# Performance work log

Measured on AMD Instinct MI355X. Metric: run time of the kernel, lower is better.

Reference implementation:

```python
import jax, jax.numpy as jnp
import numpy as np

B, C, H, W = 4, 512, 48, 48
DQ = C // 8  # inter_rate = 8
N = H * W
EPS = 1e-5


def _local_mask(radius):
    r = np.arange(N) // W
    c = np.arange(N) % W
    d = np.maximum(np.abs(r[:, None] - r[None, :]), np.abs(c[:, None] - c[None, :]))
    return jnp.asarray(d <= radius)


def setup_inputs() -> dict:
    key = jax.random.key(0)
    ks = jax.random.split(key, 12)
    def nrm(k, shape, scale=0.04):
        return jax.random.normal(k, shape, dtype=jnp.float32) * scale
    zc = jnp.zeros((C,), jnp.float32)
    oc = jnp.ones((C,), jnp.float32)
    return {
        "x": jax.random.normal(ks[0], (B, C, H, W), dtype=jnp.float32),
        "Wq": nrm(ks[1], (DQ, C)), "bq": jnp.zeros((DQ,), jnp.float32),
        "Wk": nrm(ks[2], (DQ, C)), "bk": jnp.zeros((DQ,), jnp.float32),
        "Wv": nrm(ks[3], (C, C)), "bv": zc,
        "conv1_w": nrm(ks[4], (C, C, 3, 3)),
        "bn1_w": oc, "bn1_b": zc, "bn1_m": zc, "bn1_v": oc,
        "conv2_w": nrm(ks[5], (C, C, 3, 3)),
        "bn2_w": oc, "bn2_b": zc, "bn2_m": zc, "bn2_v": oc,
        "sig1_w": nrm(ks[6], (C, C)), "sig1_b": zc,
        "sig2_w": nrm(ks[7], (C, C)), "sig2_b": zc,
        "gamma": jnp.full((1,), 0.5, jnp.float32),
        "gamma1": jnp.full((1,), 0.3, jnp.float32),
        "gamma2": jnp.full((1,), 0.2, jnp.float32),
        "mask1": _local_mask(6),
        "mask2": _local_mask(12),
    }


def _masked_softmax(e, mask):
    # exp(e)*mask / sum(exp(e)*mask) == softmax with -inf outside mask
    e = e - jnp.max(e, axis=-1, keepdims=True)
    w = jnp.exp(e) * mask.astype(e.dtype)
    return w / jnp.sum(w, axis=-1, keepdims=True)


def _conv1x1(t, w, b):
    return jnp.einsum('bchw,dc->bdhw', t, w) + b[None, :, None, None]


def _conv3x3_bn_relu(t, w, g, beta, mu, var):
    y = jax.lax.conv_general_dilated(t, w, (1, 1), 'SAME',
                                     dimension_numbers=('NCHW', 'OIHW', 'NCHW'))
    scale = (g / jnp.sqrt(var + EPS))[None, :, None, None]
    y = (y - mu[None, :, None, None]) * scale + beta[None, :, None, None]
    return jax.nn.relu(y)


def _forward(x, Wq, bq, Wk, bk, Wv, bv, conv1_w, bn1_w, bn1_b, bn1_m, bn1_v,
             conv2_w, bn2_w, bn2_b, bn2_m, bn2_v, sig1_w, sig1_b, sig2_w, sig2_b,
             gamma, gamma1, gamma2, mask1, mask2):
    b, c, h, w = x.shape
    n = h * w
    q = _conv1x1(x, Wq, bq).reshape(b, -1, n)   # [B, d, N]
    k = _conv1x1(x, Wk, bk).reshape(b, -1, n)   # [B, d, N]
    energy = jnp.einsum('bdn,bdm->bnm', q, k)   # [B, N, N] (query rows)
    a0 = jax.nn.softmax(energy, axis=-1)
    a1 = _masked_softmax(energy, mask1)
    a2 = _masked_softmax(energy, mask2)
    v = _conv1x1(x, Wv, bv).reshape(b, c, n)
    # torch: bmm(value, attention.permute(0,2,1)) -> out[b,c,m] = sum_n v[b,c,n]*a[m,n]
    out0 = jnp.einsum('bcn,bmn->bcm', v, a0).reshape(b, c, h, w)
    out0 = gamma * out0 + x
    out0 = _conv3x3_bn_relu(out0, conv1_w, bn1_w, bn1_b, bn1_m, bn1_v)
    s1 = (jax.nn.sigmoid(_conv1x1(out0, sig1_w, sig1_b)) * out0).reshape(b, c, n)
    out1 = jnp.einsum('bcn,bmn->bcm', s1, a1).reshape(b, c, h, w)
    out1 = gamma1 * out1 + out0
    out1 = _conv3x3_bn_relu(out1, conv2_w, bn2_w, bn2_b, bn2_m, bn2_v)
    s2 = (jax.nn.sigmoid(_conv1x1(out1, sig2_w, sig2_b)) * out1).reshape(b, c, n)
    out2 = jnp.einsum('bcn,bmn->bcm', s2, a2).reshape(b, c, h, w)
    return gamma2 * out2 + out1


def reference(x, Wq, bq, Wk, bk, Wv, bv, conv1_w, bn1_w, bn1_b, bn1_m, bn1_v,
              conv2_w, bn2_w, bn2_b, bn2_m, bn2_v, sig1_w, sig1_b, sig2_w, sig2_b,
              gamma, gamma1, gamma2, mask1, mask2):
    return _forward(x, Wq, bq, Wk, bk, Wv, bv, conv1_w, bn1_w, bn1_b, bn1_m, bn1_v,
                    conv2_w, bn2_w, bn2_b, bn2_m, bn2_v, sig1_w, sig1_b, sig2_w, sig2_b,
                    gamma, gamma1, gamma2, mask1, mask2)
```

## Files before the change

### kernel.cpp

```cpp
#include <hip/hip_runtime.h>
#include <math.h>

#define BB 4
#define CC 512
#define HH 48
#define WW 48
#define NN 2304
#define DDQ 64
#define LDSP 72
#define PW 50
#define PROWS 2500

typedef __attribute__((ext_vector_type(4))) float f32x4;
typedef __attribute__((ext_vector_type(8))) _Float16 half8;
typedef __attribute__((ext_vector_type(4))) _Float16 half4;
typedef __attribute__((ext_vector_type(8))) short bf16x8;

__device__ __forceinline__ int imax(int a, int b) { return a > b ? a : b; }
__device__ __forceinline__ int imin(int a, int b) { return a < b ? a : b; }
__device__ __forceinline__ int prow(int m) {
    int h = m / WW, w = m - h * WW;
    return (h + 1) * PW + (w + 1);
}
__device__ __forceinline__ unsigned short f2bf(float f) {
    unsigned u = __float_as_uint(f);
    u += 0x7fffu + ((u >> 16) & 1u);
    return (unsigned short)(u >> 16);
}
__device__ __forceinline__ float bf2f(unsigned short s) {
    unsigned u = ((unsigned)s) << 16;
    return __uint_as_float(u);
}

typedef __attribute__((address_space(1))) unsigned int g_u32;
typedef __attribute__((address_space(3))) unsigned int l_u32;
__device__ __forceinline__ void gl16(const void* g, void* l) {
    __builtin_amdgcn_global_load_lds((const g_u32*)g, (l_u32*)l, 16, 0, 0);
}

#define WAIT6()  asm volatile("s_waitcnt vmcnt(6)" ::: "memory")
#define WAIT0()  asm volatile("s_waitcnt vmcnt(0)" ::: "memory")
#define BAR()    { __builtin_amdgcn_s_barrier(); asm volatile("" ::: "memory"); }

#define BIG_DECODE()                                          \
    int raw = blockIdx.x;                                     \
    int wg = ((raw & 7) * 72) + (raw >> 3);                   \
    int jx = wg % 36; int rem = wg / 36;                      \
    int j0 = jx * 64, i0 = (rem & 3) * 128, b = rem >> 2;

#define BWAVE_IDX()                                  \
    int tid = threadIdx.x;                           \
    int wave = tid >> 6, lane = tid & 63;            \
    int wm = (wave >> 1) * 64, wn = (wave & 1) * 32; \
    int x = lane & 15, qq = lane >> 4;

__device__ __forceinline__ half8 fragld(const _Float16* T, int r, int c) {
    int kb = c ^ (r & 7);
    return *(const half8*)(T + r * 64 + kb * 8);
}
__device__ __forceinline__ bf16x8 fragld_b(const unsigned short* T, int r, int c) {
    int kb = c ^ (r & 7);
    return *(const bf16x8*)(T + r * 64 + kb * 8);
}

__device__ __forceinline__ void btile(const _Float16* As, const _Float16* Bs,
                                      f32x4 acc[4][2], int wm, int wn, int x, int qq) {
#pragma unroll
    for (int ks = 0; ks < 2; ++ks) {
        int c = ks * 4 + qq;
        half8 a0 = fragld(As, wm + x, c);
        half8 a1 = fragld(As, wm + 16 + x, c);
        half8 a2 = fragld(As, wm + 32 + x, c);
        half8 a3 = fragld(As, wm + 48 + x, c);
        half8 b0 = fragld(Bs, wn + x, c);
        half8 b1 = fragld(Bs, wn + 16 + x, c);
        acc[0][0] = __builtin_amdgcn_mfma_f32_16x16x32_f16(a0, b0, acc[0][0], 0, 0, 0);
        acc[0][1] = __builtin_amdgcn_mfma_f32_16x16x32_f16(a0, b1, acc[0][1], 0, 0, 0);
        acc[1][0] = __builtin_amdgcn_mfma_f32_16x16x32_f16(a1, b0, acc[1][0], 0, 0, 0);
        acc[1][1] = __builtin_amdgcn_mfma_f32_16x16x32_f16(a1, b1, acc[1][1], 0, 0, 0);
        acc[2][0] = __builtin_amdgcn_mfma_f32_16x16x32_f16(a2, b0, acc[2][0], 0, 0, 0);
        acc[2][1] = __builtin_amdgcn_mfma_f32_16x16x32_f16(a2, b1, acc[2][1], 0, 0, 0);
        acc[3][0] = __builtin_amdgcn_mfma_f32_16x16x32_f16(a3, b0, acc[3][0], 0, 0, 0);
        acc[3][1] = __builtin_amdgcn_mfma_f32_16x16x32_f16(a3, b1, acc[3][1], 0, 0, 0);
    }
}
__device__ __forceinline__ void btile_b(const unsigned short* As, const unsigned short* Bs,
                                        f32x4 acc[4][2], int wm, int wn, int x, int qq) {
#pragma unroll
    for (int ks = 0; ks < 2; ++ks) {
        int c = ks * 4 + qq;
        bf16x8 a0 = fragld_b(As, wm + x, c);
        bf16x8 a1 = fragld_b(As, wm + 16 + x, c);
        bf16x8 a2 = fragld_b(As, wm + 32 + x, c);
        bf16x8 a3 = fragld_b(As, wm + 48 + x, c);
        bf16x8 b0 = fragld_b(Bs, wn + x, c);
        bf16x8 b1 = fragld_b(Bs, wn + 16 + x, c);
        acc[0][0] = __builtin_amdgcn_mfma_f32_16x16x32_bf16(a0, b0, acc[0][0], 0, 0, 0);
        acc[0][1] = __builtin_amdgcn_mfma_f32_16x16x32_bf16(a0, b1, acc[0][1], 0, 0, 0);
        acc[1][0] = __builtin_amdgcn_mfma_f32_16x16x32_bf16(a1, b0, acc[1][0], 0, 0, 0);
        acc[1][1] = __builtin_amdgcn_mfma_f32_16x16x32_bf16(a1, b1, acc[1][1], 0, 0, 0);
        acc[2][0] = __builtin_amdgcn_mfma_f32_16x16x32_bf16(a2, b0, acc[2][0], 0, 0, 0);
        acc[2][1] = __builtin_amdgcn_mfma_f32_16x16x32_bf16(a2, b1, acc[2][1], 0, 0, 0);
        acc[3][0] = __builtin_amdgcn_mfma_f32_16x16x32_bf16(a3, b0, acc[3][0], 0, 0, 0);
        acc[3][1] = __builtin_amdgcn_mfma_f32_16x16x32_bf16(a3, b1, acc[3][1], 0, 0, 0);
    }
}

#define BACC_INIT()                                         \
    f32x4 zf = {0.f, 0.f, 0.f, 0.f};                        \
    f32x4 acc[4][2];                                        \
    _Pragma("unroll") for (int i_ = 0; i_ < 4; ++i_) {      \
        acc[i_][0] = zf; acc[i_][1] = zf; }

#define SLOT_A(i) int sb = (wave * 4 + (i)) * 64; int s = sb + lane; \
                  int r = s >> 3, kb = s & 7; int koff = ((kb ^ (r & 7)) << 3);
#define SLOT_B(i) int sb = (wave * 2 + (i)) * 64; int s = sb + lane; \
                  int r = s >> 3, kb = s & 7; int koff = ((kb ^ (r & 7)) << 3);

__device__ __forceinline__ void stage_rows(_Float16* dst, const _Float16* __restrict__ src,
                                           int ld, int row0, int k0, int tid) {
#pragma unroll
    for (int i = 0; i < 2; ++i) {
        int s = tid * 2 + i;
        int r = s >> 3, off = (s & 7) << 3;
        *(half8*)(dst + r * LDSP + off) =
            *(const half8*)(src + (size_t)(row0 + r) * ld + k0 + off);
    }
}
__device__ __forceinline__ void mfma_tile(const _Float16* As, const _Float16* Bs,
                                          f32x4 acc[2][2], int wm, int wn, int x, int qq) {
#pragma unroll
    for (int ks = 0; ks < 2; ++ks) {
        int kof = ks * 32 + qq * 8;
        half8 a0 = *(const half8*)(As + (wm + x) * LDSP + kof);
        half8 a1 = *(const half8*)(As + (wm + 16 + x) * LDSP + kof);
        half8 b0 = *(const half8*)(Bs + (wn + x) * LDSP + kof);
        half8 b1 = *(const half8*)(Bs + (wn + 16 + x) * LDSP + kof);
        acc[0][0] = __builtin_amdgcn_mfma_f32_16x16x32_f16(a0, b0, acc[0][0], 0, 0, 0);
        acc[0][1] = __builtin_amdgcn_mfma_f32_16x16x32_f16(a0, b1, acc[0][1], 0, 0, 0);
        acc[1][0] = __builtin_amdgcn_mfma_f32_16x16x32_f16(a1, b0, acc[1][0], 0, 0, 0);
        acc[1][1] = __builtin_amdgcn_mfma_f32_16x16x32_f16(a1, b1, acc[1][1], 0, 0, 0);
    }
}
#define WAVE_IDX()                             \
    int tid = threadIdx.x;                     \
    int wave = tid >> 6, lane = tid & 63;      \
    int wm = (wave >> 1) * 32, wn = (wave & 1) * 32; \
    int x = lane & 15, qq = lane >> 4;
#define ACC_INIT()                             \
    f32x4 zf = {0.f, 0.f, 0.f, 0.f};           \
// ... 59 lines not shown
    _Float16* outT = blockIdx.y ? kT : qT;
    const _Float16* xTb = xT + (size_t)b * NN * CC;
    ACC_INIT();
    for (int kc = 0; kc < CC; kc += 64) {
        stage_rows(As, Wp, CC, 0, kc, tid);
        stage_rows(Bs, xTb, CC, j0, kc, tid);
        __syncthreads();
        mfma_tile(As, Bs, acc, wm, wn, x, qq);
        __syncthreads();
    }
#pragma unroll
    for (int ms = 0; ms < 2; ++ms) {
        int R0 = wm + ms * 16 + qq * 4;
#pragma unroll
        for (int ns = 0; ns < 2; ++ns) {
            int Ccol = j0 + wn + ns * 16 + x;
            half4 t;
            t.x = (_Float16)(acc[ms][ns][0] + bias[R0 + 0]);
            t.y = (_Float16)(acc[ms][ns][1] + bias[R0 + 1]);
            t.z = (_Float16)(acc[ms][ns][2] + bias[R0 + 2]);
            t.w = (_Float16)(acc[ms][ns][3] + bias[R0 + 3]);
            *(half4*)(outT + ((size_t)b * NN + Ccol) * DDQ + R0) = t;
        }
    }
}

template <int EPI, int PAD>
__global__ __launch_bounds__(256) void k_cgemm(const _Float16* __restrict__ W,
                                               const float* __restrict__ bias,
                                               const _Float16* __restrict__ Bsrc,
                                               const _Float16* __restrict__ gateH,
                                               unsigned short* __restrict__ out) {
    __shared__ __align__(16) _Float16 As[2][128 * 64];
    __shared__ __align__(16) _Float16 Bs[2][64 * 64];
    BWAVE_IDX();
    BIG_DECODE();
    const _Float16* Bb = Bsrc + (size_t)b * (PAD ? (size_t)PROWS * CC : (size_t)NN * CC);

    const _Float16* aSrc[4]; int aOf[4];
#pragma unroll
    for (int i = 0; i < 4; ++i) {
        SLOT_A(i);
        aSrc[i] = W + (size_t)(i0 + r) * CC + koff;
        aOf[i] = sb * 8;
    }
    const _Float16* bSrc[2]; int bOf[2];
#pragma unroll
    for (int i = 0; i < 2; ++i) {
        SLOT_B(i);
        int row = PAD ? prow(j0 + r) : (j0 + r);
        bSrc[i] = Bb + (size_t)row * CC + koff;
        bOf[i] = sb * 8;
    }
    BACC_INIT();
#define STG_G(kc, nb)                                                          \
    { _Pragma("unroll") for (int i = 0; i < 4; ++i)                            \
          gl16(aSrc[i] + (kc), As[nb] + aOf[i]);                               \
      _Pragma("unroll") for (int i = 0; i < 2; ++i)                            \
          gl16(bSrc[i] + (kc), Bs[nb] + bOf[i]); }
    STG_G(0, 0);
    STG_G(64, 1);
    const int NSTEP = CC / 64;
#pragma unroll
    for (int t = 0; t + 2 < NSTEP; ++t) {
        WAIT6();
        BAR();
        btile(As[t & 1], Bs[t & 1], acc, wm, wn, x, qq);
        BAR();
        STG_G((t + 2) * 64, (t & 1));
    }
    WAIT6();
    BAR();
    btile(As[(NSTEP - 2) & 1], Bs[(NSTEP - 2) & 1], acc, wm, wn, x, qq);
    WAIT0();
    BAR();
    btile(As[(NSTEP - 1) & 1], Bs[(NSTEP - 1) & 1], acc, wm, wn, x, qq);
#undef STG_G
#pragma unroll
    for (int mt = 0; mt < 4; ++mt) {
        int R0 = i0 + wm + mt * 16 + qq * 4;
#pragma unroll
        for (int nt = 0; nt < 2; ++nt) {
            int Ccol = j0 + wn + nt * 16 + x;
            half4 gh;
            if (EPI == 1)
                gh = *(const half4*)(gateH + ((size_t)b * PROWS + prow(Ccol)) * CC + R0);
#pragma unroll
            for (int e = 0; e < 4; ++e) {
                float v = acc[mt][nt][e] + bias[R0 + e];
                size_t idx = ((size_t)b * CC + R0 + e) * NN + Ccol;
                if (EPI == 1) v = (float)gh[e] / (1.f + __expf(-v));
                out[idx] = f2bf(v);
            }
        }
    }
}

__global__ __launch_bounds__(256) void k_exp(const _Float16* __restrict__ qT,
                                             const _Float16* __restrict__ kT,
                                             unsigned short* __restrict__ attnB,
                                             float* __restrict__ rowsum, int rad) {
    __shared__ _Float16 qs[64 * LDSP];
    __shared__ _Float16 ks[64 * LDSP];
    __shared__ unsigned short Eh[64 * 72];
    __shared__ float psum[512];
    WAVE_IDX();
    int j0 = blockIdx.x * 64, i0 = blockIdx.y * 64, b = blockIdx.z;
    if (rad > 0) {
        int hlo = i0 / WW, hhi = (i0 + 63) / WW;
        int h2lo = imax(0, hlo - rad), h2hi = imin(HH - 1, hhi + rad);
        int klo = (h2lo * WW) & ~63;
        int khi = imin(NN, ((h2hi + 1) * WW + 63) & ~63);
        if (j0 + 64 <= klo || j0 >= khi) return;
    }
    stage_rows(qs, qT + (size_t)b * NN * DDQ, DDQ, i0, 0, tid);
    stage_rows(ks, kT + (size_t)b * NN * DDQ, DDQ, j0, 0, tid);
    __syncthreads();
    ACC_INIT();
    mfma_tile(qs, ks, acc, wm, wn, x, qq);
#pragma unroll
    for (int ns = 0; ns < 2; ++ns) {
        int col = wn + ns * 16 + x;
        int gn = j0 + col;
        int hn = gn / WW, cn = gn % WW;
#pragma unroll
        for (int ms = 0; ms < 2; ++ms)
#pragma unroll
            for (int e = 0; e < 4; ++e) {
                int row = wm + ms * 16 + qq * 4 + e;
                int gm = i0 + row;
                bool valid = true;
                if (rad > 0) {
                    int dh = gm / WW - hn; if (dh < 0) dh = -dh;
                    int dc = gm % WW - cn; if (dc < 0) dc = -dc;
                    valid = (dh <= rad) && (dc <= rad);
                }
                float w = valid ? __expf(acc[ms][ns][e]) : 0.f;
                Eh[row * 72 + col] = f2bf(w);
            }
    }
    __syncthreads();
#pragma unroll
    for (int t = 0; t < 2; ++t) {
        int s = tid + t * 256;
        int r = s >> 3, cg = (s & 7) << 3;
        bf16x8 v = *(const bf16x8*)(Eh + r * 72 + cg);
        *(bf16x8*)(attnB + ((size_t)b * NN + i0 + r) * NN + j0 + cg) = v;
        float ss = 0.f;
#pragma unroll
        for (int j = 0; j < 8; ++j) ss += bf2f((unsigned short)v[j]);
        psum[s] = ss;
    }
    __syncthreads();
    if (tid < 64) {
        float tot = 0.f;
#pragma unroll
        for (int g = 0; g < 8; ++g) tot += psum[tid * 8 + g];
        atomicAdd(rowsum + (size_t)b * NN + i0 + tid, tot);
    }
}

__global__ __launch_bounds__(256) void k_attn(const unsigned short* __restrict__ A,
                                              const unsigned short* __restrict__ attnB,
                                              const float* __restrict__ rowsum,
                                              const float* __restrict__ resF,
                                              const _Float16* __restrict__ resH,
                                              const float* __restrict__ gamma,
                                              float* __restrict__ outF,
                                              _Float16* __restrict__ outT, int rad) {
    __shared__ __align__(16) unsigned short As[2][128 * 64];
    __shared__ __align__(16) unsigned short Bs[2][64 * 64];
    BWAVE_IDX();
    BIG_DECODE();
    int klo = 0, khi = NN;
    if (rad > 0) {
        int hlo = j0 / WW, hhi = (j0 + 63) / WW;
        int h2lo = imax(0, hlo - rad), h2hi = imin(HH - 1, hhi + rad);
        klo = (h2lo * WW) & ~63;
        khi = imin(NN, ((h2hi + 1) * WW + 63) & ~63);
    }
    const unsigned short* Ab = A + (size_t)b * CC * NN;
    const unsigned short* Tb = attnB + (size_t)b * NN * NN;

    const unsigned short* aSrc[4]; int aOf[4];
#pragma unroll
    for (int i = 0; i < 4; ++i) {
        SLOT_A(i);
        aSrc[i] = Ab + (size_t)(i0 + r) * NN + koff + klo;
        aOf[i] = sb * 8;
    }
    const unsigned short* bSrc[2]; int bOf[2];
#pragma unroll
    for (int i = 0; i < 2; ++i) {
        SLOT_B(i);
        bSrc[i] = Tb + (size_t)(j0 + r) * NN + koff + klo;
        bOf[i] = sb * 8;
    }
    BACC_INIT();
    int nsteps = (khi - klo) >> 6;
#define STG_T(kc, nb)                                                          \
    { _Pragma("unroll") for (int i = 0; i < 4; ++i)                            \
          gl16(aSrc[i] + (kc), As[nb] + aOf[i]);                               \
      _Pragma("unroll") for (int i = 0; i < 2; ++i)                            \
          gl16(bSrc[i] + (kc), Bs[nb] + bOf[i]); }
    STG_T(0, 0);
    STG_T(64, 1);
    for (int t = 0; t + 2 < nsteps; ++t) {
        WAIT6();
        BAR();
        btile_b(As[t & 1], Bs[t & 1], acc, wm, wn, x, qq);
        BAR();
        STG_T((t + 2) << 6, (t & 1));
    }
    WAIT6();
    BAR();
    btile_b(As[(nsteps - 2) & 1], Bs[(nsteps - 2) & 1], acc, wm, wn, x, qq);
    WAIT0();
    BAR();
    btile_b(As[(nsteps - 1) & 1], Bs[(nsteps - 1) & 1], acc, wm, wn, x, qq);
#undef STG_T
    float g = gamma[0];
#pragma unroll
    for (int mt = 0; mt < 4; ++mt) {
        int R0 = i0 + wm + mt * 16 + qq * 4;
#pragma unroll
        for (int nt = 0; nt < 2; ++nt) {
            int Ccol = j0 + wn + nt * 16 + x;
            float linv = g / fmaxf(rowsum[(size_t)b * NN + Ccol], 1e-30f);
            float v[4];
            if (resH) {
                half4 rh = *(const half4*)(resH + ((size_t)b * PROWS + prow(Ccol)) * CC + R0);
#pragma unroll
                for (int e = 0; e < 4; ++e)
                    v[e] = acc[mt][nt][e] * linv + (float)rh[e];
            } else {
#pragma unroll
                for (int e = 0; e < 4; ++e)
                    v[e] = acc[mt][nt][e] * linv + resF[((size_t)b * CC + R0 + e) * NN + Ccol];
            }
            if (outT) {
                half4 t;
                t.x = (_Float16)v[0]; t.y = (_Float16)v[1];
                t.z = (_Float16)v[2]; t.w = (_Float16)v[3];
                *(half4*)(outT + ((size_t)b * PROWS + prow(Ccol)) * CC + R0) = t;
            }
            if (outF) {
#pragma unroll
                for (int e = 0; e < 4; ++e)
                    outF[((size_t)b * CC + R0 + e) * NN + Ccol] = v[e];
            }
        }
    }
}

__global__ __launch_bounds__(256) void k_conv3(const _Float16* __restrict__ Arep,
                                               const _Float16* __restrict__ Tpad,
                                               const float* __restrict__ bng,
                                               const float* __restrict__ bnb,
                                               const float* __restrict__ bnm,
                                               const float* __restrict__ bnv,
                                               float* __restrict__ outF,
                                               _Float16* __restrict__ outT) {
    __shared__ __align__(16) _Float16 As[2][128 * 64];
    __shared__ __align__(16) _Float16 Bs[2][64 * 64];
    BWAVE_IDX();
    BIG_DECODE();
    const _Float16* Tb = Tpad + (size_t)b * PROWS * CC;

    const _Float16* aBase[4]; int aOf[4];
#pragma unroll
    for (int i = 0; i < 4; ++i) {
        SLOT_A(i);
        aBase[i] = Arep + (size_t)(i0 + r) * CC + koff;
        aOf[i] = sb * 8;
    }
    const _Float16* bBase[2]; int bOf[2];
#pragma unroll
    for (int i = 0; i < 2; ++i) {
        SLOT_B(i);
        bBase[i] = Tb + (size_t)prow(j0 + r) * CC + koff;
        bOf[i] = sb * 8;
    }
    BACC_INIT();

#define STAGE_CONV(u, nb)                                                       \
    {                                                                           \
        int rt_ = (u) >> 3, ci_ = ((u) & 7) << 6;                               \
        int r3_ = rt_ / 3;                                                      \
        ptrdiff_t aoff_ = (ptrdiff_t)rt_ * (CC * CC) + ci_;                     \
        ptrdiff_t boff_ =                                                       \
            (ptrdiff_t)((r3_ - 1) * PW + (rt_ - r3_ * 3 - 1)) * CC + ci_;       \
        _Pragma("unroll") for (int i = 0; i < 4; ++i)                           \
            gl16(aBase[i] + aoff_, As[nb] + aOf[i]);                            \
        _Pragma("unroll") for (int i = 0; i < 2; ++i)                           \
            gl16(bBase[i] + boff_, Bs[nb] + bOf[i]);                            \
    }

    STAGE_CONV(0, 0);
    STAGE_CONV(1, 1);
    const int TOT = 9 * (CC / 64);
#pragma unroll 2
    for (int t = 0; t + 2 < TOT; ++t) {
        WAIT6();
        BAR();
        btile(As[t & 1], Bs[t & 1], acc, wm, wn, x, qq);
        BAR();
        STAGE_CONV(t + 2, (t & 1));
    }
    WAIT6();
    BAR();
    btile(As[(TOT - 2) & 1], Bs[(TOT - 2) & 1], acc, wm, wn, x, qq);
    WAIT0();
    BAR();
    btile(As[(TOT - 1) & 1], Bs[(TOT - 1) & 1], acc, wm, wn, x, qq);
#undef STAGE_CONV

#pragma unroll
    for (int mt = 0; mt < 4; ++mt) {
        int R0 = i0 + wm + mt * 16 + qq * 4;
        float sc[4], sh[4];
#pragma unroll
        for (int e = 0; e < 4; ++e) {
            sc[e] = bng[R0 + e] * rsqrtf(bnv[R0 + e] + 1e-5f);
            sh[e] = bnb[R0 + e] - bnm[R0 + e] * sc[e];
        }
#pragma unroll
        for (int nt = 0; nt < 2; ++nt) {
            int Ccol = j0 + wn + nt * 16 + x;
            float v[4];
#pragma unroll
            for (int e = 0; e < 4; ++e) {
                float t = acc[mt][nt][e] * sc[e] + sh[e];
                v[e] = t > 0.f ? t : 0.f;
            }
            if (outF) {
#pragma unroll
                for (int e = 0; e < 4; ++e)
                    outF[((size_t)b * CC + R0 + e) * NN + Ccol] = v[e];
            }
            half4 t4;
            t4.x = (_Float16)v[0]; t4.y = (_Float16)v[1];
            t4.z = (_Float16)v[2]; t4.w = (_Float16)v[3];
            *(half4*)(outT + ((size_t)b * PROWS + prow(Ccol)) * CC + R0) = t4;
        }
    }
}

extern "C" void kernel_launch(void* const* d_in, const int* in_sizes, int n_in,
                              void* d_out, int out_size, void* d_ws, size_t ws_size,
                              hipStream_t stream) {
    const float* xin  = (const float*)d_in[0];
    const float* Wq   = (const float*)d_in[1];
    const float* bq   = (const float*)d_in[2];
    const float* Wk   = (const float*)d_in[3];
    const float* bk   = (const float*)d_in[4];
    const float* Wv   = (const float*)d_in[5];
    const float* bv   = (const float*)d_in[6];
    const float* c1w  = (const float*)d_in[7];
    const float* bn1w = (const float*)d_in[8];
    const float* bn1b = (const float*)d_in[9];
    const float* bn1m = (const float*)d_in[10];
    const float* bn1v = (const float*)d_in[11];
    const float* c2w  = (const float*)d_in[12];
    const float* bn2w = (const float*)d_in[13];
    const float* bn2b = (const float*)d_in[14];
    const float* bn2m = (const float*)d_in[15];
    const float* bn2v = (const float*)d_in[16];
    const float* s1w  = (const float*)d_in[17];
    const float* s1b  = (const float*)d_in[18];
    const float* s2w  = (const float*)d_in[19];
    const float* s2b  = (const float*)d_in[20];
    const float* gamma  = (const float*)d_in[21];
    const float* gamma1 = (const float*)d_in[22];
    const float* gamma2 = (const float*)d_in[23];

    float* out = (float*)d_out;

    char* p = (char*)d_ws;
    unsigned short* attn = (unsigned short*)p; p += (size_t)BB * NN * NN * 2;
    _Float16* xT    = (_Float16*)p; p += (size_t)BB * NN * CC * 2;
    _Float16* qT    = (_Float16*)p; p += (size_t)BB * NN * DDQ * 2;
    _Float16* kT    = (_Float16*)p; p += (size_t)BB * NN * DDQ * 2;
    unsigned short* vsB = (unsigned short*)p; p += (size_t)BB * CC * NN * 2;
    _Float16* TattnP= (_Float16*)p; p += (size_t)BB * PROWS * CC * 2;
    _Float16* TconvP= (_Float16*)p; p += (size_t)BB * PROWS * CC * 2;
    float*    rR    = (float*)p;    p += (size_t)BB * CC * NN * 4;
    _Float16* wq_h  = (_Float16*)p; p += (size_t)DDQ * CC * 2;
    _Float16* wk_h  = (_Float16*)p; p += (size_t)DDQ * CC * 2;
    _Float16* wv_h  = (_Float16*)p; p += (size_t)CC * CC * 2;
    _Float16* s1_h  = (_Float16*)p; p += (size_t)CC * CC * 2;
    _Float16* s2_h  = (_Float16*)p; p += (size_t)CC * CC * 2;
    _Float16* crep1 = (_Float16*)p; p += (size_t)9 * CC * CC * 2;
    _Float16* crep2 = (_Float16*)p; p += (size_t)9 * CC * CC * 2;
    float*    rowsum= (float*)p;    p += (size_t)3 * BB * NN * 4;

    dim3 blk(256);

    hipMemsetAsync(TattnP, 0, (size_t)BB * PROWS * CC * 2, stream);
    hipMemsetAsync(TconvP, 0, (size_t)BB * PROWS * CC * 2, stream);
    hipMemsetAsync(rowsum, 0, (size_t)3 * BB * NN * 4, stream);

    k_cast_multi<<<dim3(128, 2), blk, 0, stream>>>(Wq, Wk, nullptr, wq_h, wk_h, nullptr, DDQ * CC);
    k_cast_multi<<<dim3(1024, 3), blk, 0, stream>>>(Wv, s1w, s2w, wv_h, s1_h, s2_h, CC * CC);
    k_repack_conv2<<<dim3((9 * CC * CC + 255) / 256, 2), blk, 0, stream>>>(c1w, c2w, crep1, crep2);
    k_transpose_x<<<dim3(NN / 32, CC / 32, BB), blk, 0, stream>>>(xin, xT);

    dim3 gQK(NN / 64, 2, BB);
    dim3 gExp(NN / 64, NN / 64, BB);
    dim3 gBig(576);

    float* rs0 = rowsum;
    float* rs1 = rowsum + (size_t)BB * NN;
    float* rs2 = rowsum + (size_t)2 * BB * NN;

    k_qkproj<<<gQK, blk, 0, stream>>>(wq_h, wk_h, bq, bk, xT, qT, kT);
    k_cgemm<0, 0><<<gBig, blk, 0, stream>>>(wv_h, bv, xT, nullptr, vsB);

    k_exp<<<gExp, blk, 0, stream>>>(qT, kT, attn, rs0, -1);
    k_attn<<<gBig, blk, 0, stream>>>(vsB, attn, rs0, xin, nullptr, gamma, nullptr, TattnP, -1);
    k_conv3<<<gBig, blk, 0, stream>>>(crep1, TattnP, bn1w, bn1b, bn1m, bn1v, nullptr, TconvP);

    k_cgemm<1, 1><<<gBig, blk, 0, stream>>>(s1_h, s1b, TconvP, TconvP, vsB);
    k_exp<<<gExp, blk, 0, stream>>>(qT, kT, attn, rs1, 6);
    k_attn<<<gBig, blk, 0, stream>>>(vsB, attn, rs1, nullptr, TconvP, gamma1, nullptr, TattnP, 6);
    k_conv3<<<gBig, blk, 0, stream>>>(crep2, TattnP, bn2w, bn2b, bn2m, bn2v, rR, TconvP);

    k_cgemm<1, 1><<<gBig, blk, 0, stream>>>(s2_h, s2b, TconvP, TconvP, vsB);
    k_exp<<<gExp, blk, 0, stream>>>(qT, kT, attn, rs2, 12);
    k_attn<<<gBig, blk, 0, stream>>>(vsB, attn, rs2, rR, nullptr, gamma2, out, nullptr, 12);
}
```

Baseline: 452.2 us.

## Enlarge big GEMM tiles to 128x128 per workgroup

Doubles the N dimension of the workgroup tile from 64 to 128 in the value-projection, attention-apply and 3x3 conv GEMMs, so each wave computes a 64x64 sub-tile with a 4x4 accumulator array. This raises MFMA work per LDS fragment load and halves redundant A-tile loads from global memory, but doubles B staging in LDS (64KB total) and accumulator registers. The grid drops from 576 to 288 workgroups, which may underfill the 256 CUs and reduce occupancy. The local-attention k-range bounds and the exp kernel's tile-skip logic are widened to match the larger column tiles.

```diff
diff --git a/kernel.cpp b/kernel.cpp
--- a/kernel.cpp
+++ b/kernel.cpp
@@ -38,20 +38,20 @@
     __builtin_amdgcn_global_load_lds((const g_u32*)g, (l_u32*)l, 16, 0, 0);
 }
 
-#define WAIT6()  asm volatile("s_waitcnt vmcnt(6)" ::: "memory")
+#define WAIT8()  asm volatile("s_waitcnt vmcnt(8)" ::: "memory")
 #define WAIT0()  asm volatile("s_waitcnt vmcnt(0)" ::: "memory")
 #define BAR()    { __builtin_amdgcn_s_barrier(); asm volatile("" ::: "memory"); }
 
 #define BIG_DECODE()                                          \
     int raw = blockIdx.x;                                     \
-    int wg = ((raw & 7) * 72) + (raw >> 3);                   \
-    int jx = wg % 36; int rem = wg / 36;                      \
-    int j0 = jx * 64, i0 = (rem & 3) * 128, b = rem >> 2;
+    int wg = ((raw & 7) * 36) + (raw >> 3);                   \
+    int jx = wg % 18; int rem = wg / 18;                      \
+    int j0 = jx * 128, i0 = (rem & 3) * 128, b = rem >> 2;
 
 #define BWAVE_IDX()                                  \
     int tid = threadIdx.x;                           \
     int wave = tid >> 6, lane = tid & 63;            \
-    int wm = (wave >> 1) * 64, wn = (wave & 1) * 32; \
+    int wm = (wave >> 1) * 64, wn = (wave & 1) * 64; \
     int x = lane & 15, qq = lane >> 4;
 
 __device__ __forceinline__ half8 fragld(const _Float16* T, int r, int c) {
@@ -64,58 +64,51 @@
 }
 
 __device__ __forceinline__ void btile(const _Float16* As, const _Float16* Bs,
-                                      f32x4 acc[4][2], int wm, int wn, int x, int qq) {
+                                      f32x4 acc[4][4], int wm, int wn, int x, int qq) {
 #pragma unroll
     for (int ks = 0; ks < 2; ++ks) {
         int c = ks * 4 + qq;
-        half8 a0 = fragld(As, wm + x, c);
-        half8 a1 = fragld(As, wm + 16 + x, c);
-        half8 a2 = fragld(As, wm + 32 + x, c);
-        half8 a3 = fragld(As, wm + 48 + x, c);
-        half8 b0 = fragld(Bs, wn + x, c);
-        half8 b1 = fragld(Bs, wn + 16 + x, c);
-        acc[0][0] = __builtin_amdgcn_mfma_f32_16x16x32_f16(a0, b0, acc[0][0], 0, 0, 0);
-        acc[0][1] = __builtin_amdgcn_mfma_f32_16x16x32_f16(a0, b1, acc[0][1], 0, 0, 0);
-        acc[1][0] = __builtin_amdgcn_mfma_f32_16x16x32_f16(a1, b0, acc[1][0], 0, 0, 0);
-        acc[1][1] = __builtin_amdgcn_mfma_f32_16x16x32_f16(a1, b1, acc[1][1], 0, 0, 0);
-        acc[2][0] = __builtin_amdgcn_mfma_f32_16x16x32_f16(a2, b0, acc[2][0], 0, 0, 0);
-        acc[2][1] = __builtin_amdgcn_mfma_f32_16x16x32_f16(a2, b1, acc[2][1], 0, 0, 0);
-        acc[3][0] = __builtin_amdgcn_mfma_f32_16x16x32_f16(a3, b0, acc[3][0], 0, 0, 0);
-        acc[3][1] = __builtin_amdgcn_mfma_f32_16x16x32_f16(a3, b1, acc[3][1], 0, 0, 0);
+        half8 a[4], bfr[4];
+#pragma unroll
+        for (int i = 0; i < 4; ++i) a[i] = fragld(As, wm + i * 16 + x, c);
+#pragma unroll
+        for (int i = 0; i < 4; ++i) bfr[i] = fragld(Bs, wn + i * 16 + x, c);
+#pragma unroll
+        for (int mt = 0; mt < 4; ++mt)
+#pragma unroll
+            for (int nt = 0; nt < 4; ++nt)
+                acc[mt][nt] = __builtin_amdgcn_mfma_f32_16x16x32_f16(
+                    a[mt], bfr[nt], acc[mt][nt], 0, 0, 0);
     }
 }
 __device__ __forceinline__ void btile_b(const unsigned short* As, const unsigned short* Bs,
-                                        f32x4 acc[4][2], int wm, int wn, int x, int qq) {
+                                        f32x4 acc[4][4], int wm, int wn, int x, int qq) {
 #pragma unroll
     for (int ks = 0; ks < 2; ++ks) {
         int c = ks * 4 + qq;
-        bf16x8 a0 = fragld_b(As, wm + x, c);
-        bf16x8 a1 = fragld_b(As, wm + 16 + x, c);
-        bf16x8 a2 = fragld_b(As, wm + 32 + x, c);
-        bf16x8 a3 = fragld_b(As, wm + 48 + x, c);
-        bf16x8 b0 = fragld_b(Bs, wn + x, c);
-        bf16x8 b1 = fragld_b(Bs, wn + 16 + x, c);
-        acc[0][0] = __builtin_amdgcn_mfma_f32_16x16x32_bf16(a0, b0, acc[0][0], 0, 0, 0);
-        acc[0][1] = __builtin_amdgcn_mfma_f32_16x16x32_bf16(a0, b1, acc[0][1], 0, 0, 0);
-        acc[1][0] = __builtin_amdgcn_mfma_f32_16x16x32_bf16(a1, b0, acc[1][0], 0, 0, 0);
-        acc[1][1] = __builtin_amdgcn_mfma_f32_16x16x32_bf16(a1, b1, acc[1][1], 0, 0, 0);
-        acc[2][0] = __builtin_amdgcn_mfma_f32_16x16x32_bf16(a2, b0, acc[2][0], 0, 0, 0);
-        acc[2][1] = __builtin_amdgcn_mfma_f32_16x16x32_bf16(a2, b1, acc[2][1], 0, 0, 0);
-        acc[3][0] = __builtin_amdgcn_mfma_f32_16x16x32_bf16(a3, b0, acc[3][0], 0, 0, 0);
-        acc[3][1] = __builtin_amdgcn_mfma_f32_16x16x32_bf16(a3, b1, acc[3][1], 0, 0, 0);
+        bf16x8 a[4], bfr[4];
+#pragma unroll
+        for (int i = 0; i < 4; ++i) a[i] = fragld_b(As, wm + i * 16 + x, c);
+#pragma unroll
+        for (int i = 0; i < 4; ++i) bfr[i] = fragld_b(Bs, wn + i * 16 + x, c);
+#pragma unroll
+        for (int mt = 0; mt < 4; ++mt)
+#pragma unroll
+            for (int nt = 0; nt < 4; ++nt)
+                acc[mt][nt] = __builtin_amdgcn_mfma_f32_16x16x32_bf16(
+                    a[mt], bfr[nt], acc[mt][nt], 0, 0, 0);
     }
 }
 
 #define BACC_INIT()                                         \
     f32x4 zf = {0.f, 0.f, 0.f, 0.f};                        \
-    f32x4 acc[4][2];                                        \
-    _Pragma("unroll") for (int i_ = 0; i_ < 4; ++i_) {      \
-        acc[i_][0] = zf; acc[i_][1] = zf; }
-
-#define SLOT_A(i) int sb = (wave * 4 + (i)) * 64; int s = sb + lane; \
-                  int r = s >> 3, kb = s & 7; int koff = ((kb ^ (r & 7)) << 3);
-#define SLOT_B(i) int sb = (wave * 2 + (i)) * 64; int s = sb + lane; \
-                  int r = s >> 3, kb = s & 7; int koff = ((kb ^ (r & 7)) << 3);
+    f32x4 acc[4][4];                                        \
+    _Pragma("unroll") for (int i_ = 0; i_ < 4; ++i_)        \
+        _Pragma("unroll") for (int j_ = 0; j_ < 4; ++j_)    \
+            acc[i_][j_] = zf;
+
+#define SLOT(i) int sb = (wave * 4 + (i)) * 64; int s = sb + lane; \
+                int r = s >> 3, kb = s & 7; int koff = ((kb ^ (r & 7)) << 3);
 
 __device__ __forceinline__ void stage_rows(_Float16* dst, const _Float16* __restrict__ src,
                                            int ld, int row0, int k0, int tid) {
@@ -241,7 +234,7 @@
                                                const _Float16* __restrict__ gateH,
                                                unsigned short* __restrict__ out) {
     __shared__ __align__(16) _Float16 As[2][128 * 64];
-    __shared__ __align__(16) _Float16 Bs[2][64 * 64];
+    __shared__ __align__(16) _Float16 Bs[2][128 * 64];
     BWAVE_IDX();
     BIG_DECODE();
     const _Float16* Bb = Bsrc + (size_t)b * (PAD ? (size_t)PROWS * CC : (size_t)NN * CC);
@@ -249,14 +242,14 @@
     const _Float16* aSrc[4]; int aOf[4];
 #pragma unroll
     for (int i = 0; i < 4; ++i) {
-        SLOT_A(i);
+        SLOT(i);
         aSrc[i] = W + (size_t)(i0 + r) * CC + koff;
         aOf[i] = sb * 8;
     }
-    const _Float16* bSrc[2]; int bOf[2];
-#pragma unroll
-    for (int i = 0; i < 2; ++i) {
-        SLOT_B(i);
+    const _Float16* bSrc[4]; int bOf[4];
+#pragma unroll
+    for (int i = 0; i < 4; ++i) {
+        SLOT(i);
         int row = PAD ? prow(j0 + r) : (j0 + r);
         bSrc[i] = Bb + (size_t)row * CC + koff;
         bOf[i] = sb * 8;
@@ -265,20 +258,20 @@
 #define STG_G(kc, nb)                                                          \
     { _Pragma("unroll") for (int i = 0; i < 4; ++i)                            \
           gl16(aSrc[i] + (kc), As[nb] + aOf[i]);                               \
-      _Pragma("unroll") for (int i = 0; i < 2; ++i)                            \
+      _Pragma("unroll") for (int i = 0; i < 4; ++i)                            \
           gl16(bSrc[i] + (kc), Bs[nb] + bOf[i]); }
     STG_G(0, 0);
     STG_G(64, 1);
     const int NSTEP = CC / 64;
 #pragma unroll
     for (int t = 0; t + 2 < NSTEP; ++t) {
-        WAIT6();
+        WAIT8();
         BAR();
         btile(As[t & 1], Bs[t & 1], acc, wm, wn, x, qq);
         BAR();
         STG_G((t + 2) * 64, (t & 1));
     }
-    WAIT6();
+    WAIT8();
     BAR();
     btile(As[(NSTEP - 2) & 1], Bs[(NSTEP - 2) & 1], acc, wm, wn, x, qq);
     WAIT0();
@@ -289,7 +282,7 @@
     for (int mt = 0; mt < 4; ++mt) {
         int R0 = i0 + wm + mt * 16 + qq * 4;
 #pragma unroll
-        for (int nt = 0; nt < 2; ++nt) {
+        for (int nt = 0; nt < 4; ++nt) {
             int Ccol = j0 + wn + nt * 16 + x;
             half4 gh;
             if (EPI == 1)
@@ -316,7 +309,8 @@
     WAVE_IDX();
     int j0 = blockIdx.x * 64, i0 = blockIdx.y * 64, b = blockIdx.z;
     if (rad > 0) {
-        int hlo = i0 / WW, hhi = (i0 + 63) / WW;
+        int i0b = i0 & ~127;
+        int hlo = i0b / WW, hhi = (i0b + 127) / WW;
         int h2lo = imax(0, hlo - rad), h2hi = imin(HH - 1, hhi + rad);
         int klo = (h2lo * WW) & ~63;
         int khi = imin(NN, ((h2hi + 1) * WW + 63) & ~63);
@@ -378,12 +372,12 @@
                                               float* __restrict__ outF,
                                               _Float16* __restrict__ outT, int rad) {
     __shared__ __align__(16) unsigned short As[2][128 * 64];
-    __shared__ __align__(16) unsigned short Bs[2][64 * 64];
+    __shared__ __align__(16) unsigned short Bs[2][128 * 64];
     BWAVE_IDX();
     BIG_DECODE();
     int klo = 0, khi = NN;
     if (rad > 0) {
-        int hlo = j0 / WW, hhi = (j0 + 63) / WW;
+        int hlo = j0 / WW, hhi = (j0 + 127) / WW;
         int h2lo = imax(0, hlo - rad), h2hi = imin(HH - 1, hhi + rad);
         klo = (h2lo * WW) & ~63;
         khi = imin(NN, ((h2hi + 1) * WW + 63) & ~63);
@@ -394,14 +388,14 @@
     const unsigned short* aSrc[4]; int aOf[4];
 #pragma unroll
     for (int i = 0; i < 4; ++i) {
-        SLOT_A(i);
+        SLOT(i);
         aSrc[i] = Ab + (size_t)(i0 + r) * NN + koff + klo;
         aOf[i] = sb * 8;
     }
-    const unsigned short* bSrc[2]; int bOf[2];
-#pragma unroll
-    for (int i = 0; i < 2; ++i) {
-        SLOT_B(i);
+    const unsigned short* bSrc[4]; int bOf[4];
+#pragma unroll
+    for (int i = 0; i < 4; ++i) {
+        SLOT(i);
         bSrc[i] = Tb + (size_t)(j0 + r) * NN + koff + klo;
         bOf[i] = sb * 8;
     }
@@ -410,18 +404,18 @@
 #define STG_T(kc, nb)                                                          \
     { _Pragma("unroll") for (int i = 0; i < 4; ++i)                            \
           gl16(aSrc[i] + (kc), As[nb] + aOf[i]);                               \
-      _Pragma("unroll") for (int i = 0; i < 2; ++i)                            \
+      _Pragma("unroll") for (int i = 0; i < 4; ++i)                            \
           gl16(bSrc[i] + (kc), Bs[nb] + bOf[i]); }
     STG_T(0, 0);
     STG_T(64, 1);
     for (int t = 0; t + 2 < nsteps; ++t) {
-        WAIT6();
+        WAIT8();
         BAR();
         btile_b(As[t & 1], Bs[t & 1], acc, wm, wn, x, qq);
         BAR();
         STG_T((t + 2) << 6, (t & 1));
     }
-    WAIT6();
+    WAIT8();
     BAR();
     btile_b(As[(nsteps - 2) & 1], Bs[(nsteps - 2) & 1], acc, wm, wn, x, qq);
     WAIT0();
@@ -433,7 +427,7 @@
     for (int mt = 0; mt < 4; ++mt) {
         int R0 = i0 + wm + mt * 16 + qq * 4;
 #pragma unroll
-        for (int nt = 0; nt < 2; ++nt) {
+        for (int nt = 0; nt < 4; ++nt) {
             int Ccol = j0 + wn + nt * 16 + x;
             float linv = g / fmaxf(rowsum[(size_t)b * NN + Ccol], 1e-30f);
             float v[4];
@@ -471,7 +465,7 @@
                                                float* __restrict__ outF,
                                                _Float16* __restrict__ outT) {
     __shared__ __align__(16) _Float16 As[2][128 * 64];
-    __shared__ __align__(16) _Float16 Bs[2][64 * 64];
+    __shared__ __align__(16) _Float16 Bs[2][128 * 64];
     BWAVE_IDX();
     BIG_DECODE();
     const _Float16* Tb = Tpad + (size_t)b * PROWS * CC;
@@ -479,14 +473,14 @@
     const _Float16* aBase[4]; int aOf[4];
 #pragma unroll
     for (int i = 0; i < 4; ++i) {
-        SLOT_A(i);
+        SLOT(i);
         aBase[i] = Arep + (size_t)(i0 + r) * CC + koff;
         aOf[i] = sb * 8;
     }
-    const _Float16* bBase[2]; int bOf[2];
-#pragma unroll
-    for (int i = 0; i < 2; ++i) {
-        SLOT_B(i);
+    const _Float16* bBase[4]; int bOf[4];
+#pragma unroll
+    for (int i = 0; i < 4; ++i) {
+        SLOT(i);
         bBase[i] = Tb + (size_t)prow(j0 + r) * CC + koff;
         bOf[i] = sb * 8;
     }
@@ -501,7 +495,7 @@
             (ptrdiff_t)((r3_ - 1) * PW + (rt_ - r3_ * 3 - 1)) * CC + ci_;       \
         _Pragma("unroll") for (int i = 0; i < 4; ++i)                           \
             gl16(aBase[i] + aoff_, As[nb] + aOf[i]);                            \
-        _Pragma("unroll") for (int i = 0; i < 2; ++i)                           \
+        _Pragma("unroll") for (int i = 0; i < 4; ++i)                           \
             gl16(bBase[i] + boff_, Bs[nb] + bOf[i]);                            \
     }
 
@@ -510,13 +504,13 @@
     const int TOT = 9 * (CC / 64);
 #pragma unroll 2
     for (int t = 0; t + 2 < TOT; ++t) {
-        WAIT6();
+        WAIT8();
         BAR();
         btile(As[t & 1], Bs[t & 1], acc, wm, wn, x, qq);
         BAR();
         STAGE_CONV(t + 2, (t & 1));
     }
-    WAIT6();
+    WAIT8();
     BAR();
     btile(As[(TOT - 2) & 1], Bs[(TOT - 2) & 1], acc, wm, wn, x, qq);
     WAIT0();
@@ -534,7 +528,7 @@
             sh[e] = bnb[R0 + e] - bnm[R0 + e] * sc[e];
         }
 #pragma unroll
-        for (int nt = 0; nt < 2; ++nt) {
+        for (int nt = 0; nt < 4; ++nt) {
             int Ccol = j0 + wn + nt * 16 + x;
             float v[4];
 #pragma unroll
@@ -616,7 +610,7 @@
 
     dim3 gQK(NN / 64, 2, BB);
     dim3 gExp(NN / 64, NN / 64, BB);
-    dim3 gBig(576);
+    dim3 gBig(288);
 
     float* rs0 = rowsum;
     float* rs1 = rowsum + (size_t)BB * NN;
```

Result: slower. 475.2 us (+5.1%).

## Fuse attention score exponentiation into the attention-value GEMM kernel

Applied to the files above, without the earlier changes.

Replaces the separate k_exp pass, which wrote a full B×N×N bf16 attention matrix plus atomic row sums, with a flash-style fused kernel. Each attn block recomputes the Q·K tile per step with MFMA, applies the mask and exp, stages it in LDS, and feeds it straight into the value GEMM while accumulating row sums in registers. This removes large global writes and reads of the attention matrix and the rowsum memset and atomics. In exchange, the Q·K^T work is recomputed by each channel-tile block and an extra barrier is added per step.

```diff
diff --git a/kernel.cpp b/kernel.cpp
--- a/kernel.cpp
+++ b/kernel.cpp
@@ -82,27 +82,6 @@
         acc[2][1] = __builtin_amdgcn_mfma_f32_16x16x32_f16(a2, b1, acc[2][1], 0, 0, 0);
         acc[3][0] = __builtin_amdgcn_mfma_f32_16x16x32_f16(a3, b0, acc[3][0], 0, 0, 0);
         acc[3][1] = __builtin_amdgcn_mfma_f32_16x16x32_f16(a3, b1, acc[3][1], 0, 0, 0);
-    }
-}
-__device__ __forceinline__ void btile_b(const unsigned short* As, const unsigned short* Bs,
-                                        f32x4 acc[4][2], int wm, int wn, int x, int qq) {
-#pragma unroll
-    for (int ks = 0; ks < 2; ++ks) {
-        int c = ks * 4 + qq;
-        bf16x8 a0 = fragld_b(As, wm + x, c);
-        bf16x8 a1 = fragld_b(As, wm + 16 + x, c);
-        bf16x8 a2 = fragld_b(As, wm + 32 + x, c);
-        bf16x8 a3 = fragld_b(As, wm + 48 + x, c);
-        bf16x8 b0 = fragld_b(Bs, wn + x, c);
-        bf16x8 b1 = fragld_b(Bs, wn + 16 + x, c);
-        acc[0][0] = __builtin_amdgcn_mfma_f32_16x16x32_bf16(a0, b0, acc[0][0], 0, 0, 0);
-        acc[0][1] = __builtin_amdgcn_mfma_f32_16x16x32_bf16(a0, b1, acc[0][1], 0, 0, 0);
-        acc[1][0] = __builtin_amdgcn_mfma_f32_16x16x32_bf16(a1, b0, acc[1][0], 0, 0, 0);
-        acc[1][1] = __builtin_amdgcn_mfma_f32_16x16x32_bf16(a1, b1, acc[1][1], 0, 0, 0);
-        acc[2][0] = __builtin_amdgcn_mfma_f32_16x16x32_bf16(a2, b0, acc[2][0], 0, 0, 0);
-        acc[2][1] = __builtin_amdgcn_mfma_f32_16x16x32_bf16(a2, b1, acc[2][1], 0, 0, 0);
-        acc[3][0] = __builtin_amdgcn_mfma_f32_16x16x32_bf16(a3, b0, acc[3][0], 0, 0, 0);
-        acc[3][1] = __builtin_amdgcn_mfma_f32_16x16x32_bf16(a3, b1, acc[3][1], 0, 0, 0);
     }
 }
 
@@ -305,82 +284,22 @@
     }
 }
 
-__global__ __launch_bounds__(256) void k_exp(const _Float16* __restrict__ qT,
-                                             const _Float16* __restrict__ kT,
-                                             unsigned short* __restrict__ attnB,
-                                             float* __restrict__ rowsum, int rad) {
-    __shared__ _Float16 qs[64 * LDSP];
-    __shared__ _Float16 ks[64 * LDSP];
-    __shared__ unsigned short Eh[64 * 72];
-    __shared__ float psum[512];
-    WAVE_IDX();
-    int j0 = blockIdx.x * 64, i0 = blockIdx.y * 64, b = blockIdx.z;
-    if (rad > 0) {
-        int hlo = i0 / WW, hhi = (i0 + 63) / WW;
-        int h2lo = imax(0, hlo - rad), h2hi = imin(HH - 1, hhi + rad);
-        int klo = (h2lo * WW) & ~63;
-        int khi = imin(NN, ((h2hi + 1) * WW + 63) & ~63);
-        if (j0 + 64 <= klo || j0 >= khi) return;
-    }
-    stage_rows(qs, qT + (size_t)b * NN * DDQ, DDQ, i0, 0, tid);
-    stage_rows(ks, kT + (size_t)b * NN * DDQ, DDQ, j0, 0, tid);
-    __syncthreads();
-    ACC_INIT();
-    mfma_tile(qs, ks, acc, wm, wn, x, qq);
-#pragma unroll
-    for (int ns = 0; ns < 2; ++ns) {
-        int col = wn + ns * 16 + x;
-        int gn = j0 + col;
-        int hn = gn / WW, cn = gn % WW;
-#pragma unroll
-        for (int ms = 0; ms < 2; ++ms)
-#pragma unroll
-            for (int e = 0; e < 4; ++e) {
-                int row = wm + ms * 16 + qq * 4 + e;
-                int gm = i0 + row;
-                bool valid = true;
-                if (rad > 0) {
-                    int dh = gm / WW - hn; if (dh < 0) dh = -dh;
-                    int dc = gm % WW - cn; if (dc < 0) dc = -dc;
-                    valid = (dh <= rad) && (dc <= rad);
-                }
-                float w = valid ? __expf(acc[ms][ns][e]) : 0.f;
-                Eh[row * 72 + col] = f2bf(w);
-            }
-    }
-    __syncthreads();
-#pragma unroll
-    for (int t = 0; t < 2; ++t) {
-        int s = tid + t * 256;
-        int r = s >> 3, cg = (s & 7) << 3;
-        bf16x8 v = *(const bf16x8*)(Eh + r * 72 + cg);
-        *(bf16x8*)(attnB + ((size_t)b * NN + i0 + r) * NN + j0 + cg) = v;
-        float ss = 0.f;
-#pragma unroll
-        for (int j = 0; j < 8; ++j) ss += bf2f((unsigned short)v[j]);
-        psum[s] = ss;
-    }
-    __syncthreads();
-    if (tid < 64) {
-        float tot = 0.f;
-#pragma unroll
-        for (int g = 0; g < 8; ++g) tot += psum[tid * 8 + g];
-        atomicAdd(rowsum + (size_t)b * NN + i0 + tid, tot);
-    }
-}
-
-__global__ __launch_bounds__(256) void k_attn(const unsigned short* __restrict__ A,
-                                              const unsigned short* __restrict__ attnB,
-                                              const float* __restrict__ rowsum,
-                                              const float* __restrict__ resF,
-                                              const _Float16* __restrict__ resH,
-                                              const float* __restrict__ gamma,
-                                              float* __restrict__ outF,
-                                              _Float16* __restrict__ outT, int rad) {
+__global__ __launch_bounds__(256) void k_fattn(const unsigned short* __restrict__ A,
+                                               const _Float16* __restrict__ qT,
+                                               const _Float16* __restrict__ kT,
+                                               const float* __restrict__ resF,
+                                               const _Float16* __restrict__ resH,
+                                               const float* __restrict__ gamma,
+                                               float* __restrict__ outF,
+                                               _Float16* __restrict__ outT, int rad) {
     __shared__ __align__(16) unsigned short As[2][128 * 64];
-    __shared__ __align__(16) unsigned short Bs[2][64 * 64];
+    __shared__ __align__(16) _Float16 Ks[2][64 * 64];
+    __shared__ __align__(16) unsigned short Eh[64 * 72];
+    __shared__ float rsLDS[2][64];
     BWAVE_IDX();
     BIG_DECODE();
+    int qm = (wave >> 1) * 32, qn = (wave & 1) * 32;
+
     int klo = 0, khi = NN;
     if (rad > 0) {
         int hlo = j0 / WW, hhi = (j0 + 63) / WW;
@@ -388,9 +307,9 @@
         klo = (h2lo * WW) & ~63;
         khi = imin(NN, ((h2hi + 1) * WW + 63) & ~63);
     }
+    int nsteps = (khi - klo) >> 6;
+
     const unsigned short* Ab = A + (size_t)b * CC * NN;
-    const unsigned short* Tb = attnB + (size_t)b * NN * NN;
-
     const unsigned short* aSrc[4]; int aOf[4];
 #pragma unroll
     for (int i = 0; i < 4; ++i) {
@@ -398,44 +317,147 @@
         aSrc[i] = Ab + (size_t)(i0 + r) * NN + koff + klo;
         aOf[i] = sb * 8;
     }
-    const unsigned short* bSrc[2]; int bOf[2];
+    const _Float16* kSrc[2]; int kOf[2];
 #pragma unroll
     for (int i = 0; i < 2; ++i) {
         SLOT_B(i);
-        bSrc[i] = Tb + (size_t)(j0 + r) * NN + koff + klo;
-        bOf[i] = sb * 8;
+        kSrc[i] = kT + ((size_t)b * NN + klo + r) * DDQ + koff;
+        kOf[i] = sb * 8;
+    }
+    half8 qreg[2][2];
+#pragma unroll
+    for (int ms = 0; ms < 2; ++ms)
+#pragma unroll
+        for (int ks = 0; ks < 2; ++ks)
+            qreg[ms][ks] = *(const half8*)(qT +
+                ((size_t)b * NN + j0 + qm + ms * 16 + x) * DDQ + ks * 32 + qq * 8);
+    int mh[8], mw[8];
+    if (rad > 0) {
+#pragma unroll
+        for (int idx = 0; idx < 8; ++idx) {
+            int gm = j0 + qm + (idx >> 2) * 16 + qq * 4 + (idx & 3);
+            mh[idx] = gm / WW; mw[idx] = gm - mh[idx] * WW;
+        }
     }
     BACC_INIT();
-    int nsteps = (khi - klo) >> 6;
-#define STG_T(kc, nb)                                                          \
+    float rs[2][4];
+#pragma unroll
+    for (int ms = 0; ms < 2; ++ms)
+#pragma unroll
+        for (int e = 0; e < 4; ++e) rs[ms][e] = 0.f;
+
+#define STG_F(kc, nb)                                                          \
     { _Pragma("unroll") for (int i = 0; i < 4; ++i)                            \
           gl16(aSrc[i] + (kc), As[nb] + aOf[i]);                               \
       _Pragma("unroll") for (int i = 0; i < 2; ++i)                            \
-          gl16(bSrc[i] + (kc), Bs[nb] + bOf[i]); }
-    STG_T(0, 0);
-    STG_T(64, 1);
+          gl16(kSrc[i] + ((size_t)(kc) << 6), Ks[nb] + kOf[i]); }
+#define FSTEP_BODY(nb, tt)                                                     \
+    {                                                                          \
+        f32x4 ez = {0.f, 0.f, 0.f, 0.f};                                       \
+        f32x4 eacc[2][2];                                                      \
+        eacc[0][0] = ez; eacc[0][1] = ez; eacc[1][0] = ez; eacc[1][1] = ez;    \
+        _Pragma("unroll") for (int ks = 0; ks < 2; ++ks) {                     \
+            int c = ks * 4 + qq;                                               \
+            half8 k0 = fragld(Ks[nb], qn + x, c);                              \
+            half8 k1 = fragld(Ks[nb], qn + 16 + x, c);                         \
+            eacc[0][0] = __builtin_amdgcn_mfma_f32_16x16x32_f16(               \
+                qreg[0][ks], k0, eacc[0][0], 0, 0, 0);                         \
+            eacc[0][1] = __builtin_amdgcn_mfma_f32_16x16x32_f16(               \
+                qreg[0][ks], k1, eacc[0][1], 0, 0, 0);                         \
+            eacc[1][0] = __builtin_amdgcn_mfma_f32_16x16x32_f16(               \
+                qreg[1][ks], k0, eacc[1][0], 0, 0, 0);                         \
+            eacc[1][1] = __builtin_amdgcn_mfma_f32_16x16x32_f16(               \
+                qreg[1][ks], k1, eacc[1][1], 0, 0, 0);                         \
+        }                                                                      \
+        int nbase = klo + ((tt) << 6);                                         \
+        _Pragma("unroll") for (int ns = 0; ns < 2; ++ns) {                     \
+            int col = qn + ns * 16 + x;                                        \
+            int gn = nbase + col;                                              \
+            int hn = gn / WW, cn = gn - hn * WW;                               \
+            _Pragma("unroll") for (int ms = 0; ms < 2; ++ms)                   \
+                _Pragma("unroll") for (int e = 0; e < 4; ++e) {                \
+                    int row = qm + ms * 16 + qq * 4 + e;                       \
+                    bool valid = true;                                         \
+                    if (rad > 0) {                                             \
+                        int dh = mh[ms * 4 + e] - hn; if (dh < 0) dh = -dh;    \
+                        int dc = mw[ms * 4 + e] - cn; if (dc < 0) dc = -dc;    \
+                        valid = (dh <= rad) && (dc <= rad);                    \
+                    }                                                          \
+                    float w = valid ? __expf(eacc[ms][ns][e]) : 0.f;           \
+                    unsigned short wb = f2bf(w);                               \
+                    Eh[row * 72 + col] = wb;                                   \
+                    rs[ms][e] += bf2f(wb);                                     \
+                }                                                              \
+        }                                                                      \
+        BAR();                                                                 \
+        _Pragma("unroll") for (int ks = 0; ks < 2; ++ks) {                     \
+            int c = ks * 4 + qq;                                               \
+            int kof = ks * 32 + qq * 8;                                        \
+            bf16x8 a0 = fragld_b(As[nb], wm + x, c);                           \
+            bf16x8 a1 = fragld_b(As[nb], wm + 16 + x, c);                      \
+            bf16x8 a2 = fragld_b(As[nb], wm + 32 + x, c);                      \
+            bf16x8 a3 = fragld_b(As[nb], wm + 48 + x, c);                      \
+            bf16x8 b0 = *(const bf16x8*)(Eh + (wn + x) * 72 + kof);            \
+            bf16x8 b1 = *(const bf16x8*)(Eh + (wn + 16 + x) * 72 + kof);       \
+            acc[0][0] = __builtin_amdgcn_mfma_f32_16x16x32_bf16(a0, b0, acc[0][0], 0, 0, 0); \
+            acc[0][1] = __builtin_amdgcn_mfma_f32_16x16x32_bf16(a0, b1, acc[0][1], 0, 0, 0); \
+            acc[1][0] = __builtin_amdgcn_mfma_f32_16x16x32_bf16(a1, b0, acc[1][0], 0, 0, 0); \
+            acc[1][1] = __builtin_amdgcn_mfma_f32_16x16x32_bf16(a1, b1, acc[1][1], 0, 0, 0); \
+            acc[2][0] = __builtin_amdgcn_mfma_f32_16x16x32_bf16(a2, b0, acc[2][0], 0, 0, 0); \
+            acc[2][1] = __builtin_amdgcn_mfma_f32_16x16x32_bf16(a2, b1, acc[2][1], 0, 0, 0); \
+            acc[3][0] = __builtin_amdgcn_mfma_f32_16x16x32_bf16(a3, b0, acc[3][0], 0, 0, 0); \
+            acc[3][1] = __builtin_amdgcn_mfma_f32_16x16x32_bf16(a3, b1, acc[3][1], 0, 0, 0); \
+        }                                                                      \
+    }
+
+    STG_F(0, 0);
+    STG_F(64, 1);
     for (int t = 0; t + 2 < nsteps; ++t) {
         WAIT6();
         BAR();
-        btile_b(As[t & 1], Bs[t & 1], acc, wm, wn, x, qq);
+        FSTEP_BODY((t & 1), t);
         BAR();
-        STG_T((t + 2) << 6, (t & 1));
+        STG_F((t + 2) << 6, (t & 1));
     }
     WAIT6();
     BAR();
-    btile_b(As[(nsteps - 2) & 1], Bs[(nsteps - 2) & 1], acc, wm, wn, x, qq);
+    FSTEP_BODY(((nsteps - 2) & 1), nsteps - 2);
     WAIT0();
     BAR();
-    btile_b(As[(nsteps - 1) & 1], Bs[(nsteps - 1) & 1], acc, wm, wn, x, qq);
-#undef STG_T
+    FSTEP_BODY(((nsteps - 1) & 1), nsteps - 1);
+#undef FSTEP_BODY
+#undef STG_F
+
+#pragma unroll
+    for (int ms = 0; ms < 2; ++ms)
+#pragma unroll
+        for (int e = 0; e < 4; ++e) {
+            float v = rs[ms][e];
+            v += __shfl_xor(v, 1);
+            v += __shfl_xor(v, 2);
+            v += __shfl_xor(v, 4);
+            v += __shfl_xor(v, 8);
+            rs[ms][e] = v;
+        }
+    BAR();
+    if (x == 0) {
+#pragma unroll
+        for (int ms = 0; ms < 2; ++ms)
+#pragma unroll
+            for (int e = 0; e < 4; ++e)
+                rsLDS[wave & 1][qm + ms * 16 + qq * 4 + e] = rs[ms][e];
+    }
+    BAR();
     float g = gamma[0];
 #pragma unroll
     for (int mt = 0; mt < 4; ++mt) {
         int R0 = i0 + wm + mt * 16 + qq * 4;
 #pragma unroll
         for (int nt = 0; nt < 2; ++nt) {
-            int Ccol = j0 + wn + nt * 16 + x;
-            float linv = g / fmaxf(rowsum[(size_t)b * NN + Ccol], 1e-30f);
+            int rl = wn + nt * 16 + x;
+            int Ccol = j0 + rl;
+            float rsum = rsLDS[0][rl] + rsLDS[1][rl];
+            float linv = g / fmaxf(rsum, 1e-30f);
             float v[4];
             if (resH) {
                 half4 rh = *(const half4*)(resH + ((size_t)b * PROWS + prow(Ccol)) * CC + R0);
@@ -586,7 +608,6 @@
     float* out = (float*)d_out;
 
     char* p = (char*)d_ws;
-    unsigned short* attn = (unsigned short*)p; p += (size_t)BB * NN * NN * 2;
     _Float16* xT    = (_Float16*)p; p += (size_t)BB * NN * CC * 2;
     _Float16* qT    = (_Float16*)p; p += (size_t)BB * NN * DDQ * 2;
     _Float16* kT    = (_Float16*)p; p += (size_t)BB * NN * DDQ * 2;
@@ -601,13 +622,11 @@
     _Float16* s2_h  = (_Float16*)p; p += (size_t)CC * CC * 2;
     _Float16* crep1 = (_Float16*)p; p += (size_t)9 * CC * CC * 2;
     _Float16* crep2 = (_Float16*)p; p += (size_t)9 * CC * CC * 2;
-    float*    rowsum= (float*)p;    p += (size_t)3 * BB * NN * 4;
 
     dim3 blk(256);
 
     hipMemsetAsync(TattnP, 0, (size_t)BB * PROWS * CC * 2, stream);
     hipMemsetAsync(TconvP, 0, (size_t)BB * PROWS * CC * 2, stream);
-    hipMemsetAsync(rowsum, 0, (size_t)3 * BB * NN * 4, stream);
 
     k_cast_multi<<<dim3(128, 2), blk, 0, stream>>>(Wq, Wk, nullptr, wq_h, wk_h, nullptr, DDQ * CC);
     k_cast_multi<<<dim3(1024, 3), blk, 0, stream>>>(Wv, s1w, s2w, wv_h, s1_h, s2_h, CC * CC);
@@ -615,26 +634,18 @@
     k_transpose_x<<<dim3(NN / 32, CC / 32, BB), blk, 0, stream>>>(xin, xT);
 
     dim3 gQK(NN / 64, 2, BB);
-    dim3 gExp(NN / 64, NN / 64, BB);
     dim3 gBig(576);
-
-    float* rs0 = rowsum;
-    float* rs1 = rowsum + (size_t)BB * NN;
-    float* rs2 = rowsum + (size_t)2 * BB * NN;
 
     k_qkproj<<<gQK, blk, 0, stream>>>(wq_h, wk_h, bq, bk, xT, qT, kT);
     k_cgemm<0, 0><<<gBig, blk, 0, stream>>>(wv_h, bv, xT, nullptr, vsB);
 
-    k_exp<<<gExp, blk, 0, stream>>>(qT, kT, attn, rs0, -1);
-    k_attn<<<gBig, blk, 0, stream>>>(vsB, attn, rs0, xin, nullptr, gamma, nullptr, TattnP, -1);
+    k_fattn<<<gBig, blk, 0, stream>>>(vsB, qT, kT, xin, nullptr, gamma, nullptr, TattnP, -1);
     k_conv3<<<gBig, blk, 0, stream>>>(crep1, TattnP, bn1w, bn1b, bn1m, bn1v, nullptr, TconvP);
 
     k_cgemm<1, 1><<<gBig, blk, 0, stream>>>(s1_h, s1b, TconvP, TconvP, vsB);
-    k_exp<<<gExp, blk, 0, stream>>>(qT, kT, attn, rs1, 6);
-    k_attn<<<gBig, blk, 0, stream>>>(vsB, attn, rs1, nullptr, TconvP, gamma1, nullptr, TattnP, 6);
+    k_fattn<<<gBig, blk, 0, stream>>>(vsB, qT, kT, nullptr, TconvP, gamma1, nullptr, TattnP, 6);
     k_conv3<<<gBig, blk, 0, stream>>>(crep2, TattnP, bn2w, bn2b, bn2m, bn2v, rR, TconvP);
 
     k_cgemm<1, 1><<<gBig, blk, 0, stream>>>(s2_h, s2b, TconvP, TconvP, vsB);
-    k_exp<<<gExp, blk, 0, stream>>>(qT, kT, attn, rs2, 12);
-    k_attn<<<gBig, blk, 0, stream>>>(vsB, attn, rs2, rR, nullptr, gamma2, out, nullptr, 12);
-}
+    k_fattn<<<gBig, blk, 0, stream>>>(vsB, qT, kT, rR, nullptr, gamma2, out, nullptr, 12);
+}
```

New measurement: 537.6 us. 18.9% more time.
